# Kernel optimization log

Measured on AMD Instinct MI355X. Metric: run time of the kernel, lower is better.

Reference implementation:

```python
import jax, jax.numpy as jnp
import numpy as np

DIM = 1024
HEADS = 16
DIM_HEAD = 64
NUM_FREQS = 16
INNER = HEADS * DIM_HEAD


def rotate_half(x):
    # matches torch: cat((-x[..., 1::2], x[..., ::2]), dim=-1)
    x1 = x[..., ::2]
    x2 = x[..., 1::2]
    return jnp.concatenate((-x2, x1), axis=-1)


def rope_fourier_cache(seq_len, head_dim, num_freqs):
    freqs = 10000.0 ** (-jnp.arange(0, head_dim, 2, dtype=jnp.float32) / head_dim)  # [hd/2]
    pos = jnp.arange(seq_len, dtype=jnp.float32)[:, None]  # [n,1]
    angles = pos * freqs  # [n, hd/2]
    sin = jnp.sin(angles)
    cos = jnp.cos(angles)
    # interleave-duplicate each value per pair: [n, hd]
    sin = jnp.stack([sin, sin], axis=-1).reshape(seq_len, head_dim)
    cos = jnp.stack([cos, cos], axis=-1).reshape(seq_len, head_dim)
    ffreqs = jnp.arange(1, num_freqs + 1, dtype=jnp.float32)  # [F]
    p = jnp.arange(seq_len, dtype=jnp.float32)[:, None]  # [n,1]
    fourier = jnp.concatenate([jnp.sin(p * ffreqs), jnp.cos(p * ffreqs)], axis=-1)  # [n, 2F]
    return sin, cos, fourier


def setup_inputs() -> dict:
    key = jax.random.key(0)
    ks = jax.random.split(key, 6)
    b, n = 4, 2048
    x = jax.random.normal(ks[0], (b, n, DIM), dtype=jnp.float32)
    w_qkv = jax.random.normal(ks[1], (3 * INNER, DIM), dtype=jnp.float32) * (DIM ** -0.5)
    w_fproj = jax.random.normal(ks[2], (DIM_HEAD, 2 * NUM_FREQS), dtype=jnp.float32) * ((2 * NUM_FREQS) ** -0.5)
    b_fproj = jax.random.normal(ks[3], (DIM_HEAD,), dtype=jnp.float32) * 0.02
    w_out = jax.random.normal(ks[4], (DIM, INNER), dtype=jnp.float32) * (INNER ** -0.5)
    b_out = jax.random.normal(ks[5], (DIM,), dtype=jnp.float32) * 0.02
    return {"x": x, "w_qkv": w_qkv, "w_fproj": w_fproj, "b_fproj": b_fproj,
            "w_out": w_out, "b_out": b_out}


def reference(x, w_qkv, w_fproj, b_fproj, w_out, b_out):
    b, n, _ = x.shape
    scale = DIM_HEAD ** -0.5
    qkv = x @ w_qkv.T  # [b, n, 3*inner]
    q, k, v = jnp.split(qkv, 3, axis=-1)
    def to_heads(t):
        return t.reshape(b, n, HEADS, DIM_HEAD).transpose(0, 2, 1, 3)  # [b,h,n,d]
    q, k, v = to_heads(q), to_heads(k), to_heads(v)
    sin, cos, fourier = rope_fourier_cache(n, DIM_HEAD, NUM_FREQS)
    fenc = fourier @ w_fproj.T + b_fproj  # [n, d]
    fenc = fenc[None, None]  # [1,1,n,d]
    q = q * cos + rotate_half(q) * sin + fenc
    k = k * cos + rotate_half(k) * sin + fenc
    dots = jnp.einsum('bhid,bhjd->bhij', q, k) * scale
    attn = jax.nn.softmax(dots, axis=-1)
    out = jnp.einsum('bhij,bhjd->bhid', attn, v)
    out = out.transpose(0, 2, 1, 3).reshape(b, n, INNER)
    return out @ w_out.T + b_out
```

## Files before the change

kernel.cpp:

```cpp
#include <hip/hip_runtime.h>
#include <math.h>

#define NB 4
#define SEQ 2048
#define DIMM 1024
#define NH 16
#define DHD 64
#define NFQ 16

typedef __bf16 bf16x8 __attribute__((ext_vector_type(8)));
typedef __bf16 bf16x4 __attribute__((ext_vector_type(4)));
typedef float f32x4 __attribute__((ext_vector_type(4)));

#if __has_builtin(__builtin_amdgcn_exp2f)
#define EXP2F(x) __builtin_amdgcn_exp2f(x)
#else
#define EXP2F(x) exp2f(x)
#endif

__device__ inline unsigned short f2bf(float f) {
  unsigned int u = __builtin_bit_cast(unsigned int, f);
  u += 0x7fffu + ((u >> 16) & 1u);
  return (unsigned short)(u >> 16);
}

#define GLL16(gp, lp) __builtin_amdgcn_global_load_lds( \
    (__attribute__((address_space(1))) void*)(gp), \
    (__attribute__((address_space(3))) void*)(lp), 16, 0, 0)

__global__ __launch_bounds__(64) void rope_tab_kernel(const float* __restrict__ w_fproj,
                                                      const float* __restrict__ b_fproj,
                                                      float4* __restrict__ tab) {
  const int pos = blockIdx.x;
  const int d = threadIdx.x;
  __shared__ float four[2 * NFQ];
  if (d < NFQ) {
    double a = (double)pos * (double)(d + 1);
    four[d] = (float)sin(a);
    four[d + NFQ] = (float)cos(a);
  }
  __syncthreads();
  float fe = b_fproj[d];
  const float* wr = w_fproj + d * 2 * NFQ;
#pragma unroll
  for (int j = 0; j < 2 * NFQ; ++j) fe += four[j] * wr[j];
  const int i = d >> 1;
  const double freq = exp(((double)(-2 * i)) / 64.0 * log(10000.0));
  const float angle = (float)pos * (float)freq;
  const float c = (float)cos((double)angle);
  const float s = (float)sin((double)angle);
  tab[(pos << 6) + d] = make_float4(c, s, fe, 0.f);
}

__global__ __launch_bounds__(256) void f2bf_kernel(const float* __restrict__ src,
                                                   unsigned short* __restrict__ dst, int n4) {
  for (int i = blockIdx.x * 256 + threadIdx.x; i < n4; i += gridDim.x * 256) {
    const float4 v = ((const float4*)src)[i];
    ushort4 o;
    o.x = f2bf(v.x); o.y = f2bf(v.y); o.z = f2bf(v.z); o.w = f2bf(v.w);
    ((ushort4*)dst)[i] = o;
  }
}

template<int EPI>
__global__ __launch_bounds__(256) void gemm_bt(const unsigned short* __restrict__ A,
                                               const unsigned short* __restrict__ Bw,
                                               int K,
                                               float* __restrict__ outF,
                                               unsigned short* __restrict__ outQ,
                                               unsigned short* __restrict__ outK,
                                               unsigned short* __restrict__ outV,
                                               const float4* __restrict__ tab,
                                               const float* __restrict__ bias,
                                               float qscale) {
  __shared__ __align__(16) unsigned short As[2][128 * 32];
  __shared__ __align__(16) unsigned short Bs[2][128 * 32];
  const int t = threadIdx.x, l = t & 63, w = t >> 6;
  const int wr = w >> 1, wc = w & 1;
  const int nwg = gridDim.x * gridDim.y;
  int flat = blockIdx.x + gridDim.x * blockIdx.y;
  flat = (flat & 7) * (nwg >> 3) + (flat >> 3);
  const int bm = (flat / gridDim.x) * 128, bn = (flat % gridDim.x) * 128;
  const f32x4 z = {0.f, 0.f, 0.f, 0.f};
  f32x4 acc[4][4];
#pragma unroll
  for (int m = 0; m < 4; ++m)
#pragma unroll
    for (int n = 0; n < 4; ++n) acc[m][n] = z;

  auto stage = [&](int k0, int buf) {
#pragma unroll
    for (int j = 0; j < 2; ++j) {
      const int Bb = w * 2048 + j * 1024 + l * 16;
      const int row = Bb >> 6, bin = Bb & 63;
      const int sb = bin ^ ((row & 3) << 4);
      GLL16(A  + (size_t)(bm + row) * K + k0 + (sb >> 1), (char*)(&As[buf][0]) + w * 2048 + j * 1024);
      GLL16(Bw + (size_t)(bn + row) * K + k0 + (sb >> 1), (char*)(&Bs[buf][0]) + w * 2048 + j * 1024);
    }
  };

  stage(0, 0);
  int cur = 0;
  for (int k0 = 0; k0 < K; k0 += 32) {
    __syncthreads();
    if (k0 + 32 < K) stage(k0 + 32, cur ^ 1);

    bf16x8 af[4], bfr[4];
#pragma unroll
    for (int m = 0; m < 4; ++m) {
      const int row = wr * 64 + m * 16 + (l & 15);
      const int bin = ((l >> 4) * 16) ^ ((row & 3) << 4);
      af[m] = *(const bf16x8*)((const char*)(&As[cur][0]) + row * 64 + bin);
    }
#pragma unroll
    for (int n = 0; n < 4; ++n) {
      const int row = wc * 64 + n * 16 + (l & 15);
      const int bin = ((l >> 4) * 16) ^ ((row & 3) << 4);
      bfr[n] = *(const bf16x8*)((const char*)(&Bs[cur][0]) + row * 64 + bin);
    }
#pragma unroll
    for (int m = 0; m < 4; ++m)
#pragma unroll
      for (int n = 0; n < 4; ++n)
        acc[m][n] = __builtin_amdgcn_mfma_f32_16x16x32_bf16(af[m], bfr[n], acc[m][n], 0, 0, 0);
    cur ^= 1;
  }

  const int c = l & 15;
  if (EPI == 0) {
    const int which = bn >> 10;
    const int h = ((bn & 1023) >> 6) + wc;
    if (which == 2) {
#pragma unroll
      for (int m = 0; m < 4; ++m)
#pragma unroll
        for (int n = 0; n < 4; ++n) {
          const int d = n * 16 + c;
#pragma unroll
          for (int r = 0; r < 4; ++r) {
            const int mrow = bm + wr * 64 + m * 16 + (l >> 4) * 4 + r;
            const int b = mrow >> 11, pos = mrow & (SEQ - 1);
            outV[((size_t)(b * NH + h) * DHD + d) * SEQ + pos] = f2bf(acc[m][n][r]);
          }
        }
    } else {
      unsigned short* dst = (which == 0) ? outQ : outK;
      const float sc = (which == 0) ? qscale : 1.f;
      const int laneE = (l & 48) | ((2 * c) & 15);
      const int laneO = (l & 48) | ((2 * c + 1) & 15);
      const bool hi = (c >= 8);
#pragma unroll
      for (int m = 0; m < 4; ++m)
#pragma unroll
        for (int r = 0; r < 4; ++r) {
          const int mrow = bm + wr * 64 + m * 16 + (l >> 4) * 4 + r;
          const int b = mrow >> 11, pos = mrow & (SEQ - 1);
          const float V0 = acc[m][0][r], V1 = acc[m][1][r];
          const float V2 = acc[m][2][r], V3 = acc[m][3][r];
          const float e0 = __shfl(V0, laneE), e1 = __shfl(V1, laneE);
          const float e2 = __shfl(V2, laneE), e3 = __shfl(V3, laneE);
          const float o0 = __shfl(V0, laneO), o1 = __shfl(V1, laneO);
          const float o2 = __shfl(V2, laneO), o3 = __shfl(V3, laneO);
          const float rot0 = -(hi ? o1 : o0);
          const float rot1 = -(hi ? o3 : o2);
          const float rot2 =  (hi ? e1 : e0);
          const float rot3 =  (hi ? e3 : e2);
          const float4 t0 = tab[(pos << 6) + c];
          const float4 t1 = tab[(pos << 6) + 16 + c];
          const float4 t2 = tab[(pos << 6) + 32 + c];
          const float4 t3 = tab[(pos << 6) + 48 + c];
          unsigned short* drow = dst + ((size_t)(b * NH + h) * SEQ + pos) * DHD + c;
          drow[0]  = f2bf((V0 * t0.x + rot0 * t0.y + t0.z) * sc);
          drow[16] = f2bf((V1 * t1.x + rot1 * t1.y + t1.z) * sc);
          drow[32] = f2bf((V2 * t2.x + rot2 * t2.y + t2.z) * sc);
          drow[48] = f2bf((V3 * t3.x + rot3 * t3.y + t3.z) * sc);
        }
    }
  } else {
#pragma unroll
    for (int m = 0; m < 4; ++m)
#pragma unroll
      for (int n = 0; n < 4; ++n) {
        const int ncol = bn + wc * 64 + n * 16 + c;
        const float bb = bias[ncol];
#pragma unroll
        for (int r = 0; r < 4; ++r) {
          const int mrow = bm + wr * 64 + m * 16 + (l >> 4) * 4 + r;
          outF[(size_t)mrow * DIMM + ncol] = acc[m][n][r] + bb;
        }
      }
  }
}

__global__ __launch_bounds__(256, 4) void attn_kernel(const unsigned short* __restrict__ qbf,
                                                      const unsigned short* __restrict__ kbf,
                                                      const unsigned short* __restrict__ vt,
                                                      unsigned short* __restrict__ ao) {
  __shared__ __align__(16) unsigned short Qs[64 * 64];
  __shared__ __align__(16) unsigned short Ks[2][64 * 64], Vts[2][64 * 64];
  unsigned short* Ps = Qs;
  const int t = threadIdx.x, l = t & 63, w = t >> 6, g = l >> 4;
  int flat = blockIdx.x + (blockIdx.y << 5);
  flat = (flat & 7) * 256 + (flat >> 3);
  const int q0 = (flat & 31) * 64;
  const int bh = flat >> 5;
  const int b = bh >> 4, h = bh & 15;
  const size_t hbase = (size_t)bh * SEQ * DHD;
  const f32x4 z = {0.f, 0.f, 0.f, 0.f};
  const int swz = (l & 7) << 4;
  const int qrow = w * 16 + (l & 15);

  bf16x8 ones;
#pragma unroll
  for (int j = 0; j < 8; ++j) ones[j] = (__bf16)1.0f;

  auto stageKV = [&](int kt, int buf) {
#pragma unroll
    for (int j = 0; j < 2; ++j) {
      const int Bb = w * 2048 + j * 1024 + l * 16;
      const int row = Bb >> 7, bin = Bb & 127;
      const int sb = bin ^ ((row & 7) << 4);
      GLL16(kbf + hbase + (size_t)(kt + row) * DHD + (sb >> 1),
            (char*)(&Ks[buf][0]) + w * 2048 + j * 1024);
      GLL16(vt  + hbase + (size_t)row * SEQ + kt + (sb >> 1),
            (char*)(&Vts[buf][0]) + w * 2048 + j * 1024);
    }
  };

#pragma unroll
  for (int j = 0; j < 2; ++j) {
    const int Bb = w * 2048 + j * 1024 + l * 16;
    const int row = Bb >> 7, bin = Bb & 127;
    const int sb = bin ^ ((row & 7) << 4);
    GLL16(qbf + hbase + (size_t)(q0 + row) * DHD + (sb >> 1), (char*)Qs + w * 2048 + j * 1024);
  }
  stageKV(0, 0);
  asm volatile("s_waitcnt vmcnt(4)" ::: "memory");
  bf16x8 qf[2];
#pragma unroll
  for (int ks = 0; ks < 2; ++ks)
    qf[ks] = *(const bf16x8*)((const char*)Qs + qrow * 128 + ((ks * 64 + g * 16) ^ swz));

  f32x4 of[4], lsum = z;
#pragma unroll
  for (int n = 0; n < 4; ++n) of[n] = z;

  int cur = 0;
  for (int kt = 0; kt < SEQ; kt += 64) {
    __syncthreads();
    if (kt + 64 < SEQ) stageKV(kt + 64, cur ^ 1);

    const char* Kc = (const char*)(&Ks[cur][0]);
    const char* Vc = (const char*)(&Vts[cur][0]);

    f32x4 sf[4];
#pragma unroll
    for (int n = 0; n < 4; ++n) sf[n] = z;
#pragma unroll
    for (int ks = 0; ks < 2; ++ks) {
#pragma unroll
      for (int n = 0; n < 4; ++n) {
        const int row = n * 16 + (l & 15);
        const bf16x8 kf = *(const bf16x8*)(Kc + row * 128 + ((ks * 64 + g * 16) ^ swz));
        sf[n] = __builtin_amdgcn_mfma_f32_16x16x32_bf16(kf, qf[ks], sf[n], 0, 0, 0);
      }
    }

#pragma unroll
    for (int n = 0; n < 4; ++n) {
      bf16x4 pk;
      pk[0] = (__bf16)EXP2F(sf[n][0]);
      pk[1] = (__bf16)EXP2F(sf[n][1]);
      pk[2] = (__bf16)EXP2F(sf[n][2]);
      pk[3] = (__bf16)EXP2F(sf[n][3]);
      const int byte = (n * 32 + g * 8) ^ swz;
      *(bf16x4*)((char*)Ps + qrow * 128 + byte) = pk;
    }
    bf16x8 pa[2];
#pragma unroll
    for (int ks = 0; ks < 2; ++ks)
      pa[ks] = *(const bf16x8*)((const char*)Ps + qrow * 128 + ((ks * 64 + g * 16) ^ swz));

#pragma unroll
    for (int ks = 0; ks < 2; ++ks)
      lsum = __builtin_amdgcn_mfma_f32_16x16x32_bf16(pa[ks], ones, lsum, 0, 0, 0);

#pragma unroll
    for (int nd = 0; nd < 4; ++nd) {
#pragma unroll
      for (int ks = 0; ks < 2; ++ks) {
        const int row = nd * 16 + (l & 15);
        const bf16x8 vf = *(const bf16x8*)(Vc + row * 128 + ((ks * 64 + g * 16) ^ swz));
        of[nd] = __builtin_amdgcn_mfma_f32_16x16x32_bf16(pa[ks], vf, of[nd], 0, 0, 0);
      }
    }
    cur ^= 1;
  }

#pragma unroll
  for (int r = 0; r < 4; ++r) {
    const float ir = 1.f / lsum[r];
    const int pos = q0 + w * 16 + g * 4 + r;
#pragma unroll
    for (int nd = 0; nd < 4; ++nd) {
      const int col = h * DHD + nd * 16 + (l & 15);
      ao[((size_t)(b * SEQ + pos)) * DIMM + col] = f2bf(of[nd][r] * ir);
    }
  }
}

extern "C" void kernel_launch(void* const* d_in, const int* in_sizes, int n_in,
                              void* d_out, int out_size, void* d_ws, size_t ws_size,
                              hipStream_t stream) {
  const float* x       = (const float*)d_in[0];
  const float* w_qkv   = (const float*)d_in[1];
  const float* w_fproj = (const float*)d_in[2];
  const float* b_fproj = (const float*)d_in[3];
  const float* w_out   = (const float*)d_in[4];
  const float* b_out   = (const float*)d_in[5];
  char* ws = (char*)d_ws;

  unsigned short* qbf    = (unsigned short*)(ws);
  unsigned short* kbf    = (unsigned short*)(ws + 16777216);
  unsigned short* vt     = (unsigned short*)(ws + 33554432);
  unsigned short* xbf    = (unsigned short*)(ws + 50331648);
  unsigned short* aobf   = (unsigned short*)(ws + 67108864);
  unsigned short* wqkvbf = (unsigned short*)(ws + 83886080);
  unsigned short* woutbf = (unsigned short*)(ws + 90177536);
  float4*         tab    = (float4*)(ws + 92274688);

  const float kLog2e = 1.4426950408889634f;

  hipLaunchKernelGGL(rope_tab_kernel, dim3(SEQ), dim3(DHD), 0, stream, w_fproj, b_fproj, tab);
  hipLaunchKernelGGL(f2bf_kernel, dim3(2048), dim3(256), 0, stream, x, xbf, (NB*SEQ*DIMM)/4);
  hipLaunchKernelGGL(f2bf_kernel, dim3(768), dim3(256), 0, stream, w_qkv, wqkvbf, (3*DIMM*DIMM)/4);
  hipLaunchKernelGGL(f2bf_kernel, dim3(256), dim3(256), 0, stream, w_out, woutbf, (DIMM*DIMM)/4);
  hipLaunchKernelGGL((gemm_bt<0>), dim3(24, 64), dim3(256), 0, stream,
                     xbf, wqkvbf, DIMM, (float*)nullptr, qbf, kbf, vt, tab,
                     (const float*)nullptr, 0.125f * kLog2e);
  hipLaunchKernelGGL(attn_kernel, dim3(SEQ/64, NB*NH), dim3(256), 0, stream, qbf, kbf, vt, aobf);
  hipLaunchKernelGGL((gemm_bt<1>), dim3(8, 64), dim3(256), 0, stream,
                     aobf, woutbf, DIMM, (float*)d_out, (unsigned short*)nullptr,
                     (unsigned short*)nullptr, (unsigned short*)nullptr, (const float4*)nullptr,
                     b_out, 1.0f);
}
```

Baseline: 220.0 us.

## Give each attention wave 64 query rows so K/V fragments are reused

Result: slower. 234.0 us (+6.4%).

```diff
diff --git a/kernel.cpp b/kernel.cpp
--- a/kernel.cpp
+++ b/kernel.cpp
@@ -192,23 +192,21 @@
   }
 }
 
-__global__ __launch_bounds__(256, 4) void attn_kernel(const unsigned short* __restrict__ qbf,
+__global__ __launch_bounds__(128, 2) void attn_kernel(const unsigned short* __restrict__ qbf,
                                                       const unsigned short* __restrict__ kbf,
                                                       const unsigned short* __restrict__ vt,
                                                       unsigned short* __restrict__ ao) {
-  __shared__ __align__(16) unsigned short Qs[64 * 64];
   __shared__ __align__(16) unsigned short Ks[2][64 * 64], Vts[2][64 * 64];
-  unsigned short* Ps = Qs;
-  const int t = threadIdx.x, l = t & 63, w = t >> 6, g = l >> 4;
-  int flat = blockIdx.x + (blockIdx.y << 5);
-  flat = (flat & 7) * 256 + (flat >> 3);
-  const int q0 = (flat & 31) * 64;
-  const int bh = flat >> 5;
+  __shared__ __align__(16) unsigned short Ps[2][64 * 64];
+  const int t = threadIdx.x, l = t & 63, w = t >> 6, g = l >> 4, q = l & 15;
+  int flat = blockIdx.x + (blockIdx.y << 4);
+  flat = (flat & 7) * 128 + (flat >> 3);
+  const int q0 = (flat & 15) * 128;
+  const int bh = flat >> 4;
   const int b = bh >> 4, h = bh & 15;
   const size_t hbase = (size_t)bh * SEQ * DHD;
   const f32x4 z = {0.f, 0.f, 0.f, 0.f};
-  const int swz = (l & 7) << 4;
-  const int qrow = w * 16 + (l & 15);
+  const int swz = (q & 7) << 4;
 
   bf16x8 ones;
 #pragma unroll
@@ -216,34 +214,32 @@
 
   auto stageKV = [&](int kt, int buf) {
 #pragma unroll
-    for (int j = 0; j < 2; ++j) {
-      const int Bb = w * 2048 + j * 1024 + l * 16;
-      const int row = Bb >> 7, bin = Bb & 127;
-      const int sb = bin ^ ((row & 7) << 4);
-      GLL16(kbf + hbase + (size_t)(kt + row) * DHD + (sb >> 1),
-            (char*)(&Ks[buf][0]) + w * 2048 + j * 1024);
-      GLL16(vt  + hbase + (size_t)row * SEQ + kt + (sb >> 1),
-            (char*)(&Vts[buf][0]) + w * 2048 + j * 1024);
+    for (int j = 0; j < 4; ++j) {
+      const int base = (w * 4 + j) * 1024;
+      const int row = (base + l * 16) >> 7;
+      const int sb = ((l & 7) * 16) ^ ((row & 7) << 4);
+      GLL16(kbf + hbase + (size_t)(kt + row) * DHD + (sb >> 1), (char*)(&Ks[buf][0]) + base);
+      GLL16(vt  + hbase + (size_t)row * SEQ + kt + (sb >> 1),  (char*)(&Vts[buf][0]) + base);
     }
   };
 
-#pragma unroll
-  for (int j = 0; j < 2; ++j) {
-    const int Bb = w * 2048 + j * 1024 + l * 16;
-    const int row = Bb >> 7, bin = Bb & 127;
-    const int sb = bin ^ ((row & 7) << 4);
-    GLL16(qbf + hbase + (size_t)(q0 + row) * DHD + (sb >> 1), (char*)Qs + w * 2048 + j * 1024);
-  }
+  bf16x8 qf[4][2];
+#pragma unroll
+  for (int qb = 0; qb < 4; ++qb)
+#pragma unroll
+    for (int ks = 0; ks < 2; ++ks)
+      qf[qb][ks] = *(const bf16x8*)(qbf + hbase +
+          (size_t)(q0 + w * 64 + qb * 16 + q) * DHD + ks * 32 + g * 8);
+
   stageKV(0, 0);
-  asm volatile("s_waitcnt vmcnt(4)" ::: "memory");
-  bf16x8 qf[2];
-#pragma unroll
-  for (int ks = 0; ks < 2; ++ks)
-    qf[ks] = *(const bf16x8*)((const char*)Qs + qrow * 128 + ((ks * 64 + g * 16) ^ swz));
-
-  f32x4 of[4], lsum = z;
-#pragma unroll
-  for (int n = 0; n < 4; ++n) of[n] = z;
+
+  f32x4 of[4][4], lsum[4];
+#pragma unroll
+  for (int qb = 0; qb < 4; ++qb) {
+    lsum[qb] = z;
+#pragma unroll
+    for (int nd = 0; nd < 4; ++nd) of[qb][nd] = z;
+  }
 
   int cur = 0;
   for (int kt = 0; kt < SEQ; kt += 64) {
@@ -253,60 +249,76 @@
     const char* Kc = (const char*)(&Ks[cur][0]);
     const char* Vc = (const char*)(&Vts[cur][0]);
 
-    f32x4 sf[4];
-#pragma unroll
-    for (int n = 0; n < 4; ++n) sf[n] = z;
+    f32x4 sf[4][4];
+#pragma unroll
+    for (int qb = 0; qb < 4; ++qb)
+#pragma unroll
+      for (int n = 0; n < 4; ++n) sf[qb][n] = z;
 #pragma unroll
     for (int ks = 0; ks < 2; ++ks) {
+      bf16x8 kf[4];
+#pragma unroll
+      for (int n = 0; n < 4; ++n)
+        kf[n] = *(const bf16x8*)(Kc + (n * 16 + q) * 128 + ((ks * 64 + g * 16) ^ swz));
+#pragma unroll
+      for (int qb = 0; qb < 4; ++qb)
+#pragma unroll
+        for (int n = 0; n < 4; ++n)
+          sf[qb][n] = __builtin_amdgcn_mfma_f32_16x16x32_bf16(kf[n], qf[qb][ks], sf[qb][n], 0, 0, 0);
+    }
+
+#pragma unroll
+    for (int qb = 0; qb < 4; ++qb) {
+      char* prow = (char*)(&Ps[w][0]) + (qb * 16 + q) * 128;
 #pragma unroll
       for (int n = 0; n < 4; ++n) {
-        const int row = n * 16 + (l & 15);
-        const bf16x8 kf = *(const bf16x8*)(Kc + row * 128 + ((ks * 64 + g * 16) ^ swz));
-        sf[n] = __builtin_amdgcn_mfma_f32_16x16x32_bf16(kf, qf[ks], sf[n], 0, 0, 0);
+        bf16x4 pk;
+        pk[0] = (__bf16)EXP2F(sf[qb][n][0]);
+        pk[1] = (__bf16)EXP2F(sf[qb][n][1]);
+        pk[2] = (__bf16)EXP2F(sf[qb][n][2]);
+        pk[3] = (__bf16)EXP2F(sf[qb][n][3]);
+        *(bf16x4*)(prow + ((n * 32 + g * 8) ^ swz)) = pk;
       }
     }
 
-#pragma unroll
-    for (int n = 0; n < 4; ++n) {
-      bf16x4 pk;
-      pk[0] = (__bf16)EXP2F(sf[n][0]);
-      pk[1] = (__bf16)EXP2F(sf[n][1]);
-      pk[2] = (__bf16)EXP2F(sf[n][2]);
-      pk[3] = (__bf16)EXP2F(sf[n][3]);
-      const int byte = (n * 32 + g * 8) ^ swz;
-      *(bf16x4*)((char*)Ps + qrow * 128 + byte) = pk;
-    }
-    bf16x8 pa[2];
-#pragma unroll
-    for (int ks = 0; ks < 2; ++ks)
-      pa[ks] = *(const bf16x8*)((const char*)Ps + qrow * 128 + ((ks * 64 + g * 16) ^ swz));
-
-#pragma unroll
-    for (int ks = 0; ks < 2; ++ks)
-      lsum = __builtin_amdgcn_mfma_f32_16x16x32_bf16(pa[ks], ones, lsum, 0, 0, 0);
-
-#pragma unroll
-    for (int nd = 0; nd < 4; ++nd) {
-#pragma unroll
-      for (int ks = 0; ks < 2; ++ks) {
-        const int row = nd * 16 + (l & 15);
-        const bf16x8 vf = *(const bf16x8*)(Vc + row * 128 + ((ks * 64 + g * 16) ^ swz));
-        of[nd] = __builtin_amdgcn_mfma_f32_16x16x32_bf16(pa[ks], vf, of[nd], 0, 0, 0);
+    bf16x8 vf[4][2];
+#pragma unroll
+    for (int nd = 0; nd < 4; ++nd)
+#pragma unroll
+      for (int ks = 0; ks < 2; ++ks)
+        vf[nd][ks] = *(const bf16x8*)(Vc + (nd * 16 + q) * 128 + ((ks * 64 + g * 16) ^ swz));
+
+#pragma unroll
+    for (int qb = 0; qb < 4; ++qb) {
+      const char* prow = (const char*)(&Ps[w][0]) + (qb * 16 + q) * 128;
+      bf16x8 pa[2];
+#pragma unroll
+      for (int ks = 0; ks < 2; ++ks)
+        pa[ks] = *(const bf16x8*)(prow + ((ks * 64 + g * 16) ^ swz));
+#pragma unroll
+      for (int ks = 0; ks < 2; ++ks)
+        lsum[qb] = __builtin_amdgcn_mfma_f32_16x16x32_bf16(pa[ks], ones, lsum[qb], 0, 0, 0);
+#pragma unroll
+      for (int nd = 0; nd < 4; ++nd)
+#pragma unroll
+        for (int ks = 0; ks < 2; ++ks)
+          of[qb][nd] = __builtin_amdgcn_mfma_f32_16x16x32_bf16(pa[ks], vf[nd][ks], of[qb][nd], 0, 0, 0);
+    }
+    cur ^= 1;
+  }
+
+#pragma unroll
+  for (int qb = 0; qb < 4; ++qb)
+#pragma unroll
+    for (int r = 0; r < 4; ++r) {
+      const float ir = 1.f / lsum[qb][r];
+      const int pos = q0 + w * 64 + qb * 16 + g * 4 + r;
+#pragma unroll
+      for (int nd = 0; nd < 4; ++nd) {
+        const int col = h * DHD + nd * 16 + q;
+        ao[((size_t)(b * SEQ + pos)) * DIMM + col] = f2bf(of[qb][nd][r] * ir);
       }
     }
-    cur ^= 1;
-  }
-
-#pragma unroll
-  for (int r = 0; r < 4; ++r) {
-    const float ir = 1.f / lsum[r];
-    const int pos = q0 + w * 16 + g * 4 + r;
-#pragma unroll
-    for (int nd = 0; nd < 4; ++nd) {
-      const int col = h * DHD + nd * 16 + (l & 15);
-      ao[((size_t)(b * SEQ + pos)) * DIMM + col] = f2bf(of[nd][r] * ir);
-    }
-  }
 }
 
 extern "C" void kernel_launch(void* const* d_in, const int* in_sizes, int n_in,
@@ -338,7 +350,7 @@
   hipLaunchKernelGGL((gemm_bt<0>), dim3(24, 64), dim3(256), 0, stream,
                      xbf, wqkvbf, DIMM, (float*)nullptr, qbf, kbf, vt, tab,
                      (const float*)nullptr, 0.125f * kLog2e);
-  hipLaunchKernelGGL(attn_kernel, dim3(SEQ/64, NB*NH), dim3(256), 0, stream, qbf, kbf, vt, aobf);
+  hipLaunchKernelGGL(attn_kernel, dim3(SEQ/128, NB*NH), dim3(128), 0, stream, qbf, kbf, vt, aobf);
   hipLaunchKernelGGL((gemm_bt<1>), dim3(8, 64), dim3(256), 0, stream,
                      aobf, woutbf, DIMM, (float*)d_out, (unsigned short*)nullptr,
                      (unsigned short*)nullptr, (unsigned short*)nullptr, (const float4*)nullptr,
```
